# Kernel tuning notes

Measured on AMD Instinct MI355X. Metric: run time of the kernel, lower is better.

The kernel has to match this reference:

```python
import jax, jax.numpy as jnp
import numpy as np

N_NODES = 100000


def _gcn_layer(x, src, dst, W, b, n_nodes):
    # x: [N, Cin]; src/dst already include self-loops
    h = x @ W  # [N, Cout]
    deg = jax.ops.segment_sum(jnp.ones_like(dst, dtype=h.dtype), dst,
                              num_segments=n_nodes)  # in-degree incl. self-loop
    dinv = jnp.where(deg > 0, deg ** -0.5, 0.0)
    norm = dinv[src] * dinv[dst]  # [E]
    msg = h[src] * norm[:, None]  # [E, Cout]
    out = jax.ops.segment_sum(msg, dst, num_segments=n_nodes)
    return out + b


def setup_inputs() -> dict:
    key = jax.random.key(0)
    k1, k2, k3, k4, k5, k6, k7 = jax.random.split(key, 7)
    E = 6400000
    x = jax.random.normal(k1, (N_NODES, 5), dtype=jnp.float32)
    edge_index = jax.random.randint(k2, (2, E), 0, N_NODES, dtype=jnp.int64)
    edge_f = jax.random.normal(k3, (E,), dtype=jnp.float32)
    edge_attr = jax.random.normal(k4, (E, 1), dtype=jnp.float32)
    # GCNConv params (glorot-ish scale)
    W1 = jax.random.normal(k5, (5, 8), dtype=jnp.float32) * (1.0 / np.sqrt(5))
    b1 = jnp.zeros((8,), dtype=jnp.float32)
    W2 = jax.random.normal(k6, (8, 5), dtype=jnp.float32) * (1.0 / np.sqrt(8))
    b2 = jnp.zeros((5,), dtype=jnp.float32)
    return {"x": x, "edge_index": edge_index, "edge_f": edge_f,
            "edge_attr": edge_attr, "W1": W1, "b1": b1, "W2": W2, "b2": b2}


def reference(x, edge_index, edge_f, edge_attr, W1, b1, W2, b2):
    n = x.shape[0]
    loops = jnp.arange(n, dtype=edge_index.dtype)
    src = jnp.concatenate([edge_index[0], loops])  # add self-loops (PyG default)
    dst = jnp.concatenate([edge_index[1], loops])
    h = _gcn_layer(x, src, dst, W1, b1, n)
    h = _gcn_layer(h, src, dst, W2, b2, n)
    return h
```

## Files before the change

kernel.cpp:

```cpp
#include <hip/hip_runtime.h>
#include <hip/hip_fp16.h>


#define TPB 256
#define VPB 256
#define B_BITS 8
#define MAXB 512
#define CAP 17408
#define NBLK_E 512
#define EPB 12500
#define SCT 512

typedef int int4e __attribute__((ext_vector_type(4)));
typedef _Float16 h8 __attribute__((ext_vector_type(8)));

__device__ __forceinline__ int4e ld4(const int* p) {
    return *(const int4e*)p;
}

__global__ void k_init(int B, int* __restrict__ bpos) {
    int b = blockIdx.x * blockDim.x + threadIdx.x;
    if (b < B) bpos[b] = b * CAP;
}

__global__ __launch_bounds__(SCT) void k_scat(const int* __restrict__ src,
        const int* __restrict__ dst, int E, int B,
        int* __restrict__ bpos, int* __restrict__ pairs) {
    __shared__ int sorted[EPB];
    __shared__ int hist[MAXB], scn[MAXB], cur[MAXB], gbase[MAXB];
    int t = threadIdx.x;
    for (int i = t; i < MAXB; i += SCT) hist[i] = 0;
    __syncthreads();
    int lo = blockIdx.x * EPB;
    int n = min(E - lo, EPB);
    int n4 = n & ~3;
    for (int i = t * 4; i < n4; i += SCT * 4) {
        int4e d4 = ld4(dst + lo + i);
        atomicAdd(&hist[d4.x >> B_BITS], 1);
        atomicAdd(&hist[d4.y >> B_BITS], 1);
        atomicAdd(&hist[d4.z >> B_BITS], 1);
        atomicAdd(&hist[d4.w >> B_BITS], 1);
    }
    for (int i = n4 + t; i < n; i += SCT)
        atomicAdd(&hist[dst[lo + i] >> B_BITS], 1);
    __syncthreads();
    if (t < MAXB) scn[t] = hist[t];
    __syncthreads();
    for (int off = 1; off < MAXB; off <<= 1) {
        int v = (t >= off && t < MAXB) ? scn[t - off] : 0;
        __syncthreads();
        if (t < MAXB) scn[t] += v;
        __syncthreads();
    }
    if (t < MAXB) {
        int h = hist[t];
        cur[t] = scn[t] - h;
        gbase[t] = (t < B && h) ? atomicAdd(&bpos[t], h) : 0;
    }
    __syncthreads();
    for (int i = t * 4; i < n4; i += SCT * 4) {
        int4e d4 = ld4(dst + lo + i);
        int4e s4 = ld4(src + lo + i);
        int p;
        p = atomicAdd(&cur[d4.x >> B_BITS], 1); sorted[p] = (s4.x << B_BITS) | (d4.x & (VPB - 1));
        p = atomicAdd(&cur[d4.y >> B_BITS], 1); sorted[p] = (s4.y << B_BITS) | (d4.y & (VPB - 1));
        p = atomicAdd(&cur[d4.z >> B_BITS], 1); sorted[p] = (s4.z << B_BITS) | (d4.z & (VPB - 1));
        p = atomicAdd(&cur[d4.w >> B_BITS], 1); sorted[p] = (s4.w << B_BITS) | (d4.w & (VPB - 1));
    }
    for (int i = n4 + t; i < n; i += SCT) {
        int d = dst[lo + i], s = src[lo + i];
        int p = atomicAdd(&cur[d >> B_BITS], 1);
        sorted[p] = (s << B_BITS) | (d & (VPB - 1));
    }
    __syncthreads();
    int wave = t >> 6, lane = t & 63;
    for (int bb = wave; bb < B; bb += (SCT >> 6)) {
        int h = hist[bb];
        int st = scn[bb] - h;
        int gb = gbase[bb];
        for (int j = lane; j < h; j += 64)
            pairs[gb + j] = sorted[st + j];
    }
}

__global__ __launch_bounds__(1024) void k_pre(int* __restrict__ pairs,
        const int* __restrict__ bpos, const float* __restrict__ x,
        unsigned int* __restrict__ jinfo, _Float16* __restrict__ xs, int N) {
    __shared__ int csr[CAP];
    __shared__ int hist[VPB], cur[VPB];
    __shared__ int scn[VPB];
    int t = threadIdx.x, b = blockIdx.x;
    if (t < VPB) hist[t] = 0;
    __syncthreads();
    int base = b * CAP;
    int n = bpos[b] - base, n4 = n & ~3;
    for (int i = t * 4; i < n4; i += 1024 * 4) {
        int4e p = ld4(pairs + base + i);
        atomicAdd(&hist[p.x & (VPB - 1)], 1);
        atomicAdd(&hist[p.y & (VPB - 1)], 1);
        atomicAdd(&hist[p.z & (VPB - 1)], 1);
        atomicAdd(&hist[p.w & (VPB - 1)], 1);
    }
    for (int i = n4 + t; i < n; i += 1024)
        atomicAdd(&hist[pairs[base + i] & (VPB - 1)], 1);
    __syncthreads();
    if (t < VPB) scn[t] = hist[t];
    __syncthreads();
    for (int off = 1; off < VPB; off <<= 1) {
        int v = (t >= off && t < VPB) ? scn[t - off] : 0;
        __syncthreads();
        if (t < VPB) scn[t] += v;
        __syncthreads();
    }
    int node = b * VPB + t;
    if (t < VPB) {
        int h = hist[t];
        int sl = scn[t] - h;
        cur[t] = sl;
        if (node < N) {
            jinfo[node] = ((unsigned int)(base + sl) << 9) | (unsigned int)h;
            float di = rsqrtf((float)(h + 1));
            const float* xp = x + (size_t)node * 5;
            h8 v;
            v[0] = (_Float16)(xp[0] * di); v[1] = (_Float16)(xp[1] * di);
            v[2] = (_Float16)(xp[2] * di); v[3] = (_Float16)(xp[3] * di);
            v[4] = (_Float16)(xp[4] * di);
            v[5] = (_Float16)0.f; v[6] = (_Float16)0.f; v[7] = (_Float16)0.f;
            *(h8*)(xs + (size_t)node * 8) = v;
        }
    }
    __syncthreads();
    for (int i = t * 4; i < n4; i += 1024 * 4) {
        int4e p = ld4(pairs + base + i);
        int q;
        q = atomicAdd(&cur[p.x & (VPB - 1)], 1); csr[q] = p.x >> B_BITS;
        q = atomicAdd(&cur[p.y & (VPB - 1)], 1); csr[q] = p.y >> B_BITS;
        q = atomicAdd(&cur[p.z & (VPB - 1)], 1); csr[q] = p.z >> B_BITS;
        q = atomicAdd(&cur[p.w & (VPB - 1)], 1); csr[q] = p.w >> B_BITS;
    }
    for (int i = n4 + t; i < n; i += 1024) {
        int p = pairs[base + i];
        int q = atomicAdd(&cur[p & (VPB - 1)], 1);
        csr[q] = p >> B_BITS;
    }
    __syncthreads();
    for (int i = t; i < n; i += 1024)
        pairs[base + i] = csr[i];
}

__device__ __forceinline__ void g_map(int g, int t, int* node, int* lane) {
    int q = g >> 6, r = g & 63;
    int b = q * 8 + (r & 7);
    int s = r >> 3;
    *node = b * VPB + s * 32 + (t >> 3);
    *lane = t & 7;
}

__global__ __launch_bounds__(TPB) void k_g1(const int* __restrict__ pairs,
        const unsigned int* __restrict__ jinfo, const _Float16* __restrict__ xs,
        const float* __restrict__ W1, const float* __restrict__ b1,
        const float* __restrict__ W2, _Float16* __restrict__ h2s, int N) {
    int node, lane;
    g_map(blockIdx.x, threadIdx.x, &node, &lane);
    if (node >= N) return;
    unsigned int u = jinfo[node];
    int jsa = (int)(u >> 9), cn = (int)(u & 511u);
    float a0 = 0.f, a1 = 0.f, a2 = 0.f, a3 = 0.f, a4 = 0.f;
    int j = lane;
    if (j + 24 < cn) {
        int iA = pairs[jsa + j],      iB = pairs[jsa + j + 8];
        int iC = pairs[jsa + j + 16], iD = pairs[jsa + j + 24];
        for (;;) {
            int nj = j + 32;
            bool more = (nj + 24 < cn);
            int pA, pB, pC, pD;
            if (more) {
                pA = pairs[jsa + nj];      pB = pairs[jsa + nj + 8];
                pC = pairs[jsa + nj + 16]; pD = pairs[jsa + nj + 24];
            }
            h8 vA = *(const h8*)(xs + (size_t)iA * 8);
            h8 vB = *(const h8*)(xs + (size_t)iB * 8);
            h8 vC = *(const h8*)(xs + (size_t)iC * 8);
            h8 vD = *(const h8*)(xs + (size_t)iD * 8);
            a0 += (float)vA[0] + (float)vB[0] + (float)vC[0] + (float)vD[0];
            a1 += (float)vA[1] + (float)vB[1] + (float)vC[1] + (float)vD[1];
            a2 += (float)vA[2] + (float)vB[2] + (float)vC[2] + (float)vD[2];
            a3 += (float)vA[3] + (float)vB[3] + (float)vC[3] + (float)vD[3];
            a4 += (float)vA[4] + (float)vB[4] + (float)vC[4] + (float)vD[4];
            if (!more) break;
            iA = pA; iB = pB; iC = pC; iD = pD; j = nj;
        }
        j += 32;
    }
    for (; j < cn; j += 8) {
        int sA = pairs[jsa + j];
        h8 vA = *(const h8*)(xs + (size_t)sA * 8);
        a0 += (float)vA[0]; a1 += (float)vA[1]; a2 += (float)vA[2];
        a3 += (float)vA[3]; a4 += (float)vA[4];
    }
#pragma unroll
    for (int d = 1; d < 8; d <<= 1) {
        a0 += __shfl_xor(a0, d); a1 += __shfl_xor(a1, d);
        a2 += __shfl_xor(a2, d); a3 += __shfl_xor(a3, d);
        a4 += __shfl_xor(a4, d);
    }
    float di = rsqrtf((float)(cn + 1));
    h8 sv = *(const h8*)(xs + (size_t)node * 8);
    float tc[5];
    tc[0] = a0 + (float)sv[0]; tc[1] = a1 + (float)sv[1];
    tc[2] = a2 + (float)sv[2]; tc[3] = a3 + (float)sv[3];
    tc[4] = a4 + (float)sv[4];
    float o1[8];
#pragma unroll
    for (int jj = 0; jj < 8; ++jj) {
        float h = 0.f;
#pragma unroll
        for (int c = 0; c < 5; ++c) h += tc[c] * W1[c * 8 + jj];
        o1[jj] = h * di + b1[jj];
    }
    if (lane == 0) {
        h8 w;
#pragma unroll
        for (int k = 0; k < 5; ++k) {
            float h = 0.f;
#pragma unroll
            for (int jj = 0; jj < 8; ++jj) h += o1[jj] * W2[jj * 5 + k];
            w[k] = (_Float16)(h * di);
        }
        w[5] = (_Float16)0.f; w[6] = (_Float16)0.f; w[7] = (_Float16)0.f;
        *(h8*)(h2s + (size_t)node * 8) = w;
    }
}

__global__ __launch_bounds__(TPB) void k_g2(const int* __restrict__ pairs,
        const unsigned int* __restrict__ jinfo, const _Float16* __restrict__ h2s,
        const float* __restrict__ b2, float* __restrict__ out, int N) {
    int node, lane;
    g_map(blockIdx.x, threadIdx.x, &node, &lane);
    if (node >= N) return;
    unsigned int u = jinfo[node];
    int jsa = (int)(u >> 9), cn = (int)(u & 511u);
    float a0 = 0.f, a1 = 0.f, a2 = 0.f, a3 = 0.f, a4 = 0.f;
    int j = lane;
    if (j + 24 < cn) {
        int iA = pairs[jsa + j],      iB = pairs[jsa + j + 8];
        int iC = pairs[jsa + j + 16], iD = pairs[jsa + j + 24];
        for (;;) {
            int nj = j + 32;
            bool more = (nj + 24 < cn);
            int pA, pB, pC, pD;
            if (more) {
                pA = pairs[jsa + nj];      pB = pairs[jsa + nj + 8];
                pC = pairs[jsa + nj + 16]; pD = pairs[jsa + nj + 24];
            }
            h8 vA = *(const h8*)(h2s + (size_t)iA * 8);
            h8 vB = *(const h8*)(h2s + (size_t)iB * 8);
            h8 vC = *(const h8*)(h2s + (size_t)iC * 8);
            h8 vD = *(const h8*)(h2s + (size_t)iD * 8);
            a0 += (float)vA[0] + (float)vB[0] + (float)vC[0] + (float)vD[0];
            a1 += (float)vA[1] + (float)vB[1] + (float)vC[1] + (float)vD[1];
            a2 += (float)vA[2] + (float)vB[2] + (float)vC[2] + (float)vD[2];
            a3 += (float)vA[3] + (float)vB[3] + (float)vC[3] + (float)vD[3];
            a4 += (float)vA[4] + (float)vB[4] + (float)vC[4] + (float)vD[4];
            if (!more) break;
            iA = pA; iB = pB; iC = pC; iD = pD; j = nj;
        }
        j += 32;
    }
    for (; j < cn; j += 8) {
        int sA = pairs[jsa + j];
        h8 vA = *(const h8*)(h2s + (size_t)sA * 8);
        a0 += (float)vA[0]; a1 += (float)vA[1]; a2 += (float)vA[2];
        a3 += (float)vA[3]; a4 += (float)vA[4];
    }
#pragma unroll
    for (int d = 1; d < 8; d <<= 1) {
        a0 += __shfl_xor(a0, d); a1 += __shfl_xor(a1, d);
        a2 += __shfl_xor(a2, d); a3 += __shfl_xor(a3, d);
        a4 += __shfl_xor(a4, d);
    }
    if (lane == 0) {
        float di = rsqrtf((float)(cn + 1));
        h8 sv = *(const h8*)(h2s + (size_t)node * 8);
        float* op = out + (size_t)node * 5;
        op[0] = (a0 + (float)sv[0]) * di + b2[0];
        op[1] = (a1 + (float)sv[1]) * di + b2[1];
        op[2] = (a2 + (float)sv[2]) * di + b2[2];
        op[3] = (a3 + (float)sv[3]) * di + b2[3];
        op[4] = (a4 + (float)sv[4]) * di + b2[4];
    }
}

extern "C" void kernel_launch(void* const* d_in, const int* in_sizes, int n_in,
                              void* d_out, int out_size, void* d_ws, size_t ws_size,
                              hipStream_t stream) {
    const float* x   = (const float*)d_in[0];
    const int*  eidx = (const int*)d_in[1];
    const float* W1 = (const float*)d_in[4];
    const float* b1 = (const float*)d_in[5];
    const float* W2 = (const float*)d_in[6];
    const float* b2 = (const float*)d_in[7];
    float* out = (float*)d_out;

    const int N = in_sizes[0] / 5;
    const int E = in_sizes[1] / 2;
    const int* src = eidx;
    const int* dst = eidx + E;

    const int B = (N + VPB - 1) / VPB;

    int*      pairs = (int*)d_ws;
    _Float16* xs    = (_Float16*)(pairs + (size_t)B * CAP);
    _Float16* h2s   = xs + (size_t)8 * N;
    unsigned int* jinfo = (unsigned int*)(h2s + (size_t)8 * N);
    int*      bpos  = (int*)(jinfo + N);

    const int gG = ((B + 7) / 8) * 64;

    k_init <<<(B + TPB - 1) / TPB, TPB, 0, stream>>>(B, bpos);
    k_scat <<<NBLK_E, SCT, 0, stream>>>(src, dst, E, B, bpos, pairs);
    k_pre  <<<B, 1024, 0, stream>>>(pairs, bpos, x, jinfo, xs, N);
    k_g1   <<<gG, TPB, 0, stream>>>(pairs, jinfo, xs, W1, b1, W2, h2s, N);
    k_g2   <<<gG, TPB, 0, stream>>>(pairs, jinfo, h2s, b2, out, N);
}
```

Before: 227.4 us.

## Split degree pass from CSR build and fuse CSR build with layer-1 gather

The preprocessing kernel is split in two. A lighter kernel now only computes per-node degrees, jinfo and the prescaled fp16 features, because the gather needs every node's xs ready. A second 1024-thread kernel builds the per-bucket CSR in shared memory, writes it back for layer 2, and runs the layer-1 aggregation straight from shared-memory indices with four lanes per node. This drops the separate k_g1 launch and its global reread of the neighbor indices, but it adds a second histogram pass over pairs and ties the gather to one block per 256-node bucket with less parallelism per node.

```diff
diff --git a/kernel.cpp b/kernel.cpp
--- a/kernel.cpp
+++ b/kernel.cpp
@@ -10,6 +10,7 @@
 #define NBLK_E 512
 #define EPB 12500
 #define SCT 512
+#define DGT 512
 
 typedef int int4e __attribute__((ext_vector_type(4)));
 typedef _Float16 h8 __attribute__((ext_vector_type(8)));
@@ -83,25 +84,24 @@
     }
 }
 
-__global__ __launch_bounds__(1024) void k_pre(int* __restrict__ pairs,
+__global__ __launch_bounds__(DGT) void k_pre(const int* __restrict__ pairs,
         const int* __restrict__ bpos, const float* __restrict__ x,
         unsigned int* __restrict__ jinfo, _Float16* __restrict__ xs, int N) {
-    __shared__ int csr[CAP];
-    __shared__ int hist[VPB], cur[VPB];
+    __shared__ int hist[VPB];
     __shared__ int scn[VPB];
     int t = threadIdx.x, b = blockIdx.x;
     if (t < VPB) hist[t] = 0;
     __syncthreads();
     int base = b * CAP;
     int n = bpos[b] - base, n4 = n & ~3;
-    for (int i = t * 4; i < n4; i += 1024 * 4) {
+    for (int i = t * 4; i < n4; i += DGT * 4) {
         int4e p = ld4(pairs + base + i);
         atomicAdd(&hist[p.x & (VPB - 1)], 1);
         atomicAdd(&hist[p.y & (VPB - 1)], 1);
         atomicAdd(&hist[p.z & (VPB - 1)], 1);
         atomicAdd(&hist[p.w & (VPB - 1)], 1);
     }
-    for (int i = n4 + t; i < n; i += 1024)
+    for (int i = n4 + t; i < n; i += DGT)
         atomicAdd(&hist[pairs[base + i] & (VPB - 1)], 1);
     __syncthreads();
     if (t < VPB) scn[t] = hist[t];
@@ -113,23 +113,42 @@
         __syncthreads();
     }
     int node = b * VPB + t;
+    if (t < VPB && node < N) {
+        int h = hist[t];
+        int start = base + scn[t] - h;
+        jinfo[node] = ((unsigned int)start << 9) | (unsigned int)h;
+        float di = rsqrtf((float)(h + 1));
+        const float* xp = x + (size_t)node * 5;
+        h8 v;
+        v[0] = (_Float16)(xp[0] * di); v[1] = (_Float16)(xp[1] * di);
+        v[2] = (_Float16)(xp[2] * di); v[3] = (_Float16)(xp[3] * di);
+        v[4] = (_Float16)(xp[4] * di);
+        v[5] = (_Float16)0.f; v[6] = (_Float16)0.f; v[7] = (_Float16)0.f;
+        *(h8*)(xs + (size_t)node * 8) = v;
+    }
+}
+
+__global__ __launch_bounds__(1024) void k_ag1(int* __restrict__ pairs,
+        const int* __restrict__ bpos, const unsigned int* __restrict__ jinfo,
+        const _Float16* __restrict__ xs, const float* __restrict__ b1,
+        const float* __restrict__ W1, const float* __restrict__ W2,
+        _Float16* __restrict__ h2s, int N) {
+    __shared__ int csr[CAP];
+    __shared__ int js[VPB], ct[VPB], cur[VPB];
+    int t = threadIdx.x, b = blockIdx.x;
+    int base = b * CAP;
     if (t < VPB) {
-        int h = hist[t];
-        int sl = scn[t] - h;
-        cur[t] = sl;
+        int node = b * VPB + t;
+        int s = 0, c = 0;
         if (node < N) {
-            jinfo[node] = ((unsigned int)(base + sl) << 9) | (unsigned int)h;
-            float di = rsqrtf((float)(h + 1));
-            const float* xp = x + (size_t)node * 5;
-            h8 v;
-            v[0] = (_Float16)(xp[0] * di); v[1] = (_Float16)(xp[1] * di);
-            v[2] = (_Float16)(xp[2] * di); v[3] = (_Float16)(xp[3] * di);
-            v[4] = (_Float16)(xp[4] * di);
-            v[5] = (_Float16)0.f; v[6] = (_Float16)0.f; v[7] = (_Float16)0.f;
-            *(h8*)(xs + (size_t)node * 8) = v;
+            unsigned int u = jinfo[node];
+            s = (int)(u >> 9) - base;
+            c = (int)(u & 511u);
         }
-    }
-    __syncthreads();
+        js[t] = s; ct[t] = c; cur[t] = s;
+    }
+    __syncthreads();
+    int n = bpos[b] - base, n4 = n & ~3;
     for (int i = t * 4; i < n4; i += 1024 * 4) {
         int4e p = ld4(pairs + base + i);
         int q;
@@ -146,6 +165,68 @@
     __syncthreads();
     for (int i = t; i < n; i += 1024)
         pairs[base + i] = csr[i];
+    int lane = t & 3, ln = t >> 2;
+    int node = b * VPB + ln;
+    if (node >= N) return;
+    int s0 = js[ln], cn = ct[ln];
+    float a0 = 0.f, a1 = 0.f, a2 = 0.f, a3 = 0.f, a4 = 0.f;
+    int j = lane;
+    for (; j + 12 < cn; j += 16) {
+        int sA = csr[s0 + j];
+        int sB = csr[s0 + j + 4];
+        int sC = csr[s0 + j + 8];
+        int sD = csr[s0 + j + 12];
+        h8 vA = *(const h8*)(xs + (size_t)sA * 8);
+        h8 vB = *(const h8*)(xs + (size_t)sB * 8);
+        h8 vC = *(const h8*)(xs + (size_t)sC * 8);
+        h8 vD = *(const h8*)(xs + (size_t)sD * 8);
+        a0 += (float)vA[0] + (float)vB[0] + (float)vC[0] + (float)vD[0];
+        a1 += (float)vA[1] + (float)vB[1] + (float)vC[1] + (float)vD[1];
+        a2 += (float)vA[2] + (float)vB[2] + (float)vC[2] + (float)vD[2];
+        a3 += (float)vA[3] + (float)vB[3] + (float)vC[3] + (float)vD[3];
+        a4 += (float)vA[4] + (float)vB[4] + (float)vC[4] + (float)vD[4];
+    }
+    for (; j < cn; j += 4) {
+        int sA = csr[s0 + j];
+        h8 vA = *(const h8*)(xs + (size_t)sA * 8);
+        a0 += (float)vA[0]; a1 += (float)vA[1]; a2 += (float)vA[2];
+        a3 += (float)vA[3]; a4 += (float)vA[4];
+    }
+#pragma unroll
+    for (int d = 1; d < 4; d <<= 1) {
+        a0 += __shfl_xor(a0, d); a1 += __shfl_xor(a1, d);
+        a2 += __shfl_xor(a2, d); a3 += __shfl_xor(a3, d);
+        a4 += __shfl_xor(a4, d);
+    }
+    h8 sv = *(const h8*)(xs + (size_t)node * 8);
+    float tc[5];
+    tc[0] = a0 + (float)sv[0]; tc[1] = a1 + (float)sv[1];
+    tc[2] = a2 + (float)sv[2]; tc[3] = a3 + (float)sv[3];
+    tc[4] = a4 + (float)sv[4];
+    float di = rsqrtf((float)(cn + 1));
+    float o1[8];
+#pragma unroll
+    for (int jj = 0; jj < 8; ++jj) {
+        float h = 0.f;
+#pragma unroll
+        for (int c = 0; c < 5; ++c) h += tc[c] * W1[c * 8 + jj];
+        o1[jj] = h * di + b1[jj];
+    }
+    if (lane == 0) {
+        float hv[5];
+#pragma unroll
+        for (int k = 0; k < 5; ++k) {
+            float h = 0.f;
+#pragma unroll
+            for (int jj = 0; jj < 8; ++jj) h += o1[jj] * W2[jj * 5 + k];
+            hv[k] = h * di;
+        }
+        h8 w;
+        w[0] = (_Float16)hv[0]; w[1] = (_Float16)hv[1]; w[2] = (_Float16)hv[2];
+        w[3] = (_Float16)hv[3]; w[4] = (_Float16)hv[4];
+        w[5] = (_Float16)0.f; w[6] = (_Float16)0.f; w[7] = (_Float16)0.f;
+        *(h8*)(h2s + (size_t)node * 8) = w;
+    }
 }
 
 __device__ __forceinline__ void g_map(int g, int t, int* node, int* lane) {
@@ -154,82 +235,6 @@
     int s = r >> 3;
     *node = b * VPB + s * 32 + (t >> 3);
     *lane = t & 7;
-}
-
-__global__ __launch_bounds__(TPB) void k_g1(const int* __restrict__ pairs,
-        const unsigned int* __restrict__ jinfo, const _Float16* __restrict__ xs,
-        const float* __restrict__ W1, const float* __restrict__ b1,
-        const float* __restrict__ W2, _Float16* __restrict__ h2s, int N) {
-    int node, lane;
-    g_map(blockIdx.x, threadIdx.x, &node, &lane);
-    if (node >= N) return;
-    unsigned int u = jinfo[node];
-    int jsa = (int)(u >> 9), cn = (int)(u & 511u);
-    float a0 = 0.f, a1 = 0.f, a2 = 0.f, a3 = 0.f, a4 = 0.f;
-    int j = lane;
-    if (j + 24 < cn) {
-        int iA = pairs[jsa + j],      iB = pairs[jsa + j + 8];
-        int iC = pairs[jsa + j + 16], iD = pairs[jsa + j + 24];
-        for (;;) {
-            int nj = j + 32;
-            bool more = (nj + 24 < cn);
-            int pA, pB, pC, pD;
-            if (more) {
-                pA = pairs[jsa + nj];      pB = pairs[jsa + nj + 8];
-                pC = pairs[jsa + nj + 16]; pD = pairs[jsa + nj + 24];
-            }
-            h8 vA = *(const h8*)(xs + (size_t)iA * 8);
-            h8 vB = *(const h8*)(xs + (size_t)iB * 8);
-            h8 vC = *(const h8*)(xs + (size_t)iC * 8);
-            h8 vD = *(const h8*)(xs + (size_t)iD * 8);
-            a0 += (float)vA[0] + (float)vB[0] + (float)vC[0] + (float)vD[0];
-            a1 += (float)vA[1] + (float)vB[1] + (float)vC[1] + (float)vD[1];
-            a2 += (float)vA[2] + (float)vB[2] + (float)vC[2] + (float)vD[2];
-            a3 += (float)vA[3] + (float)vB[3] + (float)vC[3] + (float)vD[3];
-            a4 += (float)vA[4] + (float)vB[4] + (float)vC[4] + (float)vD[4];
-            if (!more) break;
-            iA = pA; iB = pB; iC = pC; iD = pD; j = nj;
-        }
-        j += 32;
-    }
-    for (; j < cn; j += 8) {
-        int sA = pairs[jsa + j];
-        h8 vA = *(const h8*)(xs + (size_t)sA * 8);
-        a0 += (float)vA[0]; a1 += (float)vA[1]; a2 += (float)vA[2];
-        a3 += (float)vA[3]; a4 += (float)vA[4];
-    }
-#pragma unroll
-    for (int d = 1; d < 8; d <<= 1) {
-        a0 += __shfl_xor(a0, d); a1 += __shfl_xor(a1, d);
-        a2 += __shfl_xor(a2, d); a3 += __shfl_xor(a3, d);
-        a4 += __shfl_xor(a4, d);
-    }
-    float di = rsqrtf((float)(cn + 1));
-    h8 sv = *(const h8*)(xs + (size_t)node * 8);
-    float tc[5];
-    tc[0] = a0 + (float)sv[0]; tc[1] = a1 + (float)sv[1];
-    tc[2] = a2 + (float)sv[2]; tc[3] = a3 + (float)sv[3];
-    tc[4] = a4 + (float)sv[4];
-    float o1[8];
-#pragma unroll
-    for (int jj = 0; jj < 8; ++jj) {
-        float h = 0.f;
-#pragma unroll
-        for (int c = 0; c < 5; ++c) h += tc[c] * W1[c * 8 + jj];
-        o1[jj] = h * di + b1[jj];
-    }
-    if (lane == 0) {
-        h8 w;
-#pragma unroll
-        for (int k = 0; k < 5; ++k) {
-            float h = 0.f;
-#pragma unroll
-            for (int jj = 0; jj < 8; ++jj) h += o1[jj] * W2[jj * 5 + k];
-            w[k] = (_Float16)(h * di);
-        }
-        w[5] = (_Float16)0.f; w[6] = (_Float16)0.f; w[7] = (_Float16)0.f;
-        *(h8*)(h2s + (size_t)node * 8) = w;
-    }
 }
 
 __global__ __launch_bounds__(TPB) void k_g2(const int* __restrict__ pairs,
@@ -319,7 +324,7 @@
 
     k_init <<<(B + TPB - 1) / TPB, TPB, 0, stream>>>(B, bpos);
     k_scat <<<NBLK_E, SCT, 0, stream>>>(src, dst, E, B, bpos, pairs);
-    k_pre  <<<B, 1024, 0, stream>>>(pairs, bpos, x, jinfo, xs, N);
-    k_g1   <<<gG, TPB, 0, stream>>>(pairs, jinfo, xs, W1, b1, W2, h2s, N);
+    k_pre  <<<B, DGT, 0, stream>>>(pairs, bpos, x, jinfo, xs, N);
+    k_ag1  <<<B, 1024, 0, stream>>>(pairs, bpos, jinfo, xs, b1, W1, W2, h2s, N);
     k_g2   <<<gG, TPB, 0, stream>>>(pairs, jinfo, h2s, b2, out, N);
 }
```

Result: no change. 225.1 us (-1.0%).
